# Kernel tuning notes

Hardware: AMD Instinct MI355X
Metric: run time of the kernel (lower is better)

Reference implementation:

```python
import jax, jax.numpy as jnp
import numpy as np

TEMPERATURE = 1.0

N = 20000  # = subsample, so the random-subsample branch is not taken


def setup_inputs() -> dict:
    key = jax.random.key(0)
    k1, k2 = jax.random.split(key)
    logits = jax.random.normal(k1, (N,), dtype=jnp.float32)
    targets = jax.random.uniform(k2, (N,), dtype=jnp.float32)  # relevance in [0,1]
    return {"logits": logits, "targets": targets}


def reference(logits, targets):
    s = logits.reshape(-1)
    y = targets.reshape(-1)
    n = s.shape[0]
    t = jnp.asarray(TEMPERATURE, dtype=s.dtype)

    # diff[i, j] = s[j] - s[i]; approx rank of item j = 1 + sum_i sigmoid((s[j]-s[i])/T)
    diff = s[None, :] - s[:, None]                     # [n, n]
    approx_rank = jax.nn.sigmoid(diff / t).sum(axis=0) + 1.0

    discount = 1.0 / jnp.log2(approx_rank + 1.0)
    dcg = jnp.sum(y * discount)

    ideal_rank = jnp.arange(1, n + 1, dtype=s.dtype)
    ideal_discount = 1.0 / jnp.log2(ideal_rank + 1.0)
    sorted_y = jnp.sort(y)[::-1]                        # descending
    idcg = jnp.sum(sorted_y * ideal_discount)

    ndcg = dcg / (idcg + 1e-8)
    loss = 1.0 - ndcg
    # early-return guard: if total relevance < 1, loss is 0
    return jnp.where(jnp.sum(y) < 1.0, jnp.zeros((), dtype=s.dtype), loss)
```

## Files before the change

kernel.cpp:

```cpp
#include <hip/hip_runtime.h>
#include <hip/hip_bf16.h>


#define LOG2E 1.442695040888963387f
#define M_NODES 64
#define XHALF 8.0
#define NB 2048
#define PI_D 3.14159265358979323846
#define BT 1024

#if __has_builtin(__builtin_amdgcn_exp2f)
#define EXP2(x) __builtin_amdgcn_exp2f(x)
#else
#define EXP2(x) exp2f(x)
#endif

#if __has_builtin(__builtin_amdgcn_rcpf)
#define RCP(x) __builtin_amdgcn_rcpf(x)
#else
#define RCP(x) (1.0f / (x))
#endif

#define OFF_ACC    0
#define OFF_DONE   32
#define OFF_PREFIX 64
#define OFF_NODES  8320
#define OFF_YBKT   8832

__device__ __forceinline__ int bucket_of(float y) {
  int b = (int)(y * (float)NB);
  return b < 0 ? 0 : (b > NB - 1 ? NB - 1 : b);
}

__global__ __launch_bounds__(BT) void produce_kernel(
    const float* __restrict__ s, const float* __restrict__ y,
    char* __restrict__ ws, int n) {
  const int tid = threadIdx.x;
  double* acc = (double*)(ws + OFF_ACC);
  int* done = (int*)(ws + OFF_DONE);
  int* prefix = (int*)(ws + OFF_PREFIX);
  float2* nodes = (float2*)(ws + OFF_NODES);
  float* ybkt = (float*)(ws + OFF_YBKT);

  if (blockIdx.x == 0) {
    __shared__ int hist[NB];
    __shared__ int part[BT];
    for (int b = tid; b < NB; b += BT) hist[b] = 0;
    __syncthreads();

    const float4* y4 = (const float4*)y;
    const int n4 = n >> 2;
    for (int i = tid; i < n4; i += BT) {
      const float4 v = y4[i];
      atomicAdd(&hist[bucket_of(v.x)], 1);
      atomicAdd(&hist[bucket_of(v.y)], 1);
      atomicAdd(&hist[bucket_of(v.z)], 1);
      atomicAdd(&hist[bucket_of(v.w)], 1);
    }
    for (int i = (n4 << 2) + tid; i < n; i += BT)
      atomicAdd(&hist[bucket_of(y[i])], 1);
    __syncthreads();

    const int base = tid * 2;
    const int l0 = hist[base], l1 = hist[base + 1];
    const int sum2 = l0 + l1;
    part[tid] = sum2;
    __syncthreads();
    for (int off = 1; off < BT; off <<= 1) {
      const int v = (tid >= off) ? part[tid - off] : 0;
      __syncthreads();
      part[tid] += v;
      __syncthreads();
    }
    const int run = part[tid] - sum2;
    prefix[base] = run;
    prefix[base + 1] = run + l0;
    if (tid == BT - 1) prefix[NB] = run + sum2;
    __syncthreads();
    hist[base] = run;
    hist[base + 1] = run + l0;
    __syncthreads();

    for (int i = tid; i < n4; i += BT) {
      const float4 v = y4[i];
      ybkt[atomicAdd(&hist[bucket_of(v.x)], 1)] = v.x;
      ybkt[atomicAdd(&hist[bucket_of(v.y)], 1)] = v.y;
      ybkt[atomicAdd(&hist[bucket_of(v.z)], 1)] = v.z;
      ybkt[atomicAdd(&hist[bucket_of(v.w)], 1)] = v.w;
    }
    for (int i = (n4 << 2) + tid; i < n; i += BT) {
      const float yv = y[i];
      ybkt[atomicAdd(&hist[bucket_of(yv)], 1)] = yv;
    }
  } else {
    const int k = blockIdx.x - 1;
    if (k == 0 && tid < 4) {
      if (tid < 3) acc[tid] = 0.0;
      else *done = 0;
    }
    const float xk =
        (float)(XHALF * cos(PI_D * (double)k / (double)(M_NODES - 1)));
    double F = 0.0;
    const float4* s4 = (const float4*)s;
    const int n4 = n >> 2;
    for (int i = tid; i < n4; i += BT) {
      const float4 v = s4[i];
      float t = RCP(1.0f + EXP2((v.x - xk) * LOG2E));
      t += RCP(1.0f + EXP2((v.y - xk) * LOG2E));
      t += RCP(1.0f + EXP2((v.z - xk) * LOG2E));
      t += RCP(1.0f + EXP2((v.w - xk) * LOG2E));
      F += (double)t;
    }
    for (int i = (n4 << 2) + tid; i < n; i += BT)
      F += (double)RCP(1.0f + EXP2((s[i] - xk) * LOG2E));
    for (int off = 32; off > 0; off >>= 1) F += __shfl_down(F, off);
    __shared__ double wsum[BT / 64];
    if ((tid & 63) == 0) wsum[tid >> 6] = F;
    __syncthreads();
    if (tid == 0) {
      double t = 0.0;
#pragma unroll
      for (int w = 0; w < BT / 64; ++w) t += wsum[w];
      nodes[k] = make_float2(xk, (float)t);
    }
  }
}

__global__ __launch_bounds__(256) void consume_kernel(
    const float* __restrict__ s, const float* __restrict__ y,
    char* __restrict__ ws, float* __restrict__ out, int n, int nblocks) {
  double* acc = (double*)(ws + OFF_ACC);
  int* done = (int*)(ws + OFF_DONE);
  const int* prefix = (const int*)(ws + OFF_PREFIX);
  const float2* nodes = (const float2*)(ws + OFF_NODES);
  const float* ybkt = (const float*)(ws + OFF_YBKT);

  __shared__ float2 nd[M_NODES];
  __shared__ double wsum[12];
  const int tid = threadIdx.x;
  if (tid < M_NODES) nd[tid] = nodes[tid];
  __syncthreads();

  const int j = blockIdx.x * 256 + tid;
  double dc = 0.0, ic = 0.0, ys = 0.0;
  if (j < n) {
    const float x = s[j];
    const float yj = y[j];
    double num = 0.0, den = 0.0;
    int hit = -1;
#pragma unroll
    for (int k = 0; k < M_NODES; ++k) {
      const float d = x - nd[k].x;
      float w = (k & 1) ? -1.0f : 1.0f;
      if (k == 0 || k == M_NODES - 1) w *= 0.5f;
      if (d == 0.0f) {
        hit = k;
      } else {
        const float iv = w * RCP(d);
        num += (double)iv * (double)nd[k].y;
        den += (double)iv;
      }
    }
    const double F = (hit >= 0) ? (double)nd[hit].y : (num / den);

    const int b = bucket_of(yj);
    const int s1 = prefix[b + 1];
    int cnt = n - s1;
    for (int t = prefix[b]; t < s1; ++t) cnt += (ybkt[t] > yj);

    dc = (double)yj / log2(F + 2.0);
    ic = (double)yj / log2((double)cnt + 2.0);
    ys = (double)yj;
  }
  for (int off = 32; off > 0; off >>= 1) {
    dc += __shfl_down(dc, off);
    ic += __shfl_down(ic, off);
    ys += __shfl_down(ys, off);
  }
  const int wv = tid >> 6;
  if ((tid & 63) == 0) {
    wsum[wv] = dc;
    wsum[wv + 4] = ic;
    wsum[wv + 8] = ys;
  }
  __syncthreads();
  if (tid == 0) {
    atomicAdd(&acc[0], wsum[0] + wsum[1] + wsum[2] + wsum[3]);
    atomicAdd(&acc[1], wsum[4] + wsum[5] + wsum[6] + wsum[7]);
    atomicAdd(&acc[2], wsum[8] + wsum[9] + wsum[10] + wsum[11]);
    __threadfence();
    const int old = atomicAdd(done, 1);
    if (old == nblocks - 1) {
      const double dcg = atomicAdd(&acc[0], 0.0);
      const double idcg = atomicAdd(&acc[1], 0.0);
      const double ysum = atomicAdd(&acc[2], 0.0);
      const double loss = 1.0 - dcg / (idcg + 1e-8);
      out[0] = (ysum < 1.0) ? 0.0f : (float)loss;
    }
  }
}

extern "C" void kernel_launch(void* const* d_in, const int* in_sizes, int n_in,
                              void* d_out, int out_size, void* d_ws, size_t ws_size,
                              hipStream_t stream) {
  const float* s = (const float*)d_in[0];
  const float* y = (const float*)d_in[1];
  const int n = in_sizes[0];
  char* wsb = (char*)d_ws;

  const int nb = (n + 255) / 256;
  produce_kernel<<<M_NODES + 1, BT, 0, stream>>>(s, y, wsb, n);
  consume_kernel<<<nb, 256, 0, stream>>>(s, y, wsb, (float*)d_out, n, nb);
}
```

Baseline: 82.61 us.

## Fuse produce and consume kernels with a software grid barrier

Merges the two launches into one kernel of 65 blocks of 1024 threads that meet at a global atomic spin barrier. After the barrier, each block computes NDCG terms for 1024 items, reading node values and the bucketed histogram through relaxed atomic loads. Workspace state moves into device globals, which the last block resets for the next call. This removes one kernel launch and the gap between launches. The barrier relies on all 65 blocks being co-resident, and the consume phase now only covers n up to 65*1024 items.

```diff
diff --git a/kernel.cpp b/kernel.cpp
--- a/kernel.cpp
+++ b/kernel.cpp
@@ -1,5 +1,4 @@
 #include <hip/hip_runtime.h>
-#include <hip/hip_bf16.h>
 
 
 #define LOG2E 1.442695040888963387f
@@ -8,6 +7,8 @@
 #define NB 2048
 #define PI_D 3.14159265358979323846
 #define BT 1024
+#define GBLKS (M_NODES + 1)
+#define MAXN 131072
 
 #if __has_builtin(__builtin_amdgcn_exp2f)
 #define EXP2(x) __builtin_amdgcn_exp2f(x)
@@ -21,30 +22,38 @@
 #define RCP(x) (1.0f / (x))
 #endif
 
-#define OFF_ACC    0
-#define OFF_DONE   32
-#define OFF_PREFIX 64
-#define OFF_NODES  8320
-#define OFF_YBKT   8832
+__device__ double g_acc[3] = {0.0, 0.0, 0.0};
+__device__ int g_done = 0;
+__device__ int g_bar = 0;
+__device__ int g_prefix[NB + 1];
+__device__ float g_nodex[M_NODES];
+__device__ float g_nodef[M_NODES];
+__device__ float g_ybkt[MAXN];
 
 __device__ __forceinline__ int bucket_of(float y) {
   int b = (int)(y * (float)NB);
   return b < 0 ? 0 : (b > NB - 1 ? NB - 1 : b);
 }
 
-__global__ __launch_bounds__(BT) void produce_kernel(
+__device__ __forceinline__ float aloadf(const float* p) {
+  return __hip_atomic_load(p, __ATOMIC_RELAXED, __HIP_MEMORY_SCOPE_AGENT);
+}
+__device__ __forceinline__ int aloadi(const int* p) {
+  return __hip_atomic_load(p, __ATOMIC_RELAXED, __HIP_MEMORY_SCOPE_AGENT);
+}
+
+__global__ __launch_bounds__(BT) void fused_kernel(
     const float* __restrict__ s, const float* __restrict__ y,
-    char* __restrict__ ws, int n) {
+    float* __restrict__ out, int n) {
   const int tid = threadIdx.x;
-  double* acc = (double*)(ws + OFF_ACC);
-  int* done = (int*)(ws + OFF_DONE);
-  int* prefix = (int*)(ws + OFF_PREFIX);
-  float2* nodes = (float2*)(ws + OFF_NODES);
-  float* ybkt = (float*)(ws + OFF_YBKT);
-
-  if (blockIdx.x == 0) {
-    __shared__ int hist[NB];
-    __shared__ int part[BT];
+  const int blk = blockIdx.x;
+
+  __shared__ int hist[NB];
+  __shared__ int part[BT];
+  __shared__ double wsum[48];
+  __shared__ float2 nd[M_NODES];
+
+  if (blk == 0) {
     for (int b = tid; b < NB; b += BT) hist[b] = 0;
     __syncthreads();
 
@@ -73,9 +82,9 @@
       __syncthreads();
     }
     const int run = part[tid] - sum2;
-    prefix[base] = run;
-    prefix[base + 1] = run + l0;
-    if (tid == BT - 1) prefix[NB] = run + sum2;
+    g_prefix[base] = run;
+    g_prefix[base + 1] = run + l0;
+    if (tid == BT - 1) g_prefix[NB] = run + sum2;
     __syncthreads();
     hist[base] = run;
     hist[base + 1] = run + l0;
@@ -83,21 +92,17 @@
 
     for (int i = tid; i < n4; i += BT) {
       const float4 v = y4[i];
-      ybkt[atomicAdd(&hist[bucket_of(v.x)], 1)] = v.x;
-      ybkt[atomicAdd(&hist[bucket_of(v.y)], 1)] = v.y;
-      ybkt[atomicAdd(&hist[bucket_of(v.z)], 1)] = v.z;
-      ybkt[atomicAdd(&hist[bucket_of(v.w)], 1)] = v.w;
+      g_ybkt[atomicAdd(&hist[bucket_of(v.x)], 1)] = v.x;
+      g_ybkt[atomicAdd(&hist[bucket_of(v.y)], 1)] = v.y;
+      g_ybkt[atomicAdd(&hist[bucket_of(v.z)], 1)] = v.z;
+      g_ybkt[atomicAdd(&hist[bucket_of(v.w)], 1)] = v.w;
     }
     for (int i = (n4 << 2) + tid; i < n; i += BT) {
       const float yv = y[i];
-      ybkt[atomicAdd(&hist[bucket_of(yv)], 1)] = yv;
+      g_ybkt[atomicAdd(&hist[bucket_of(yv)], 1)] = yv;
     }
   } else {
-    const int k = blockIdx.x - 1;
-    if (k == 0 && tid < 4) {
-      if (tid < 3) acc[tid] = 0.0;
-      else *done = 0;
-    }
+    const int k = blk - 1;
     const float xk =
         (float)(XHALF * cos(PI_D * (double)k / (double)(M_NODES - 1)));
     double F = 0.0;
@@ -114,34 +119,31 @@
     for (int i = (n4 << 2) + tid; i < n; i += BT)
       F += (double)RCP(1.0f + EXP2((s[i] - xk) * LOG2E));
     for (int off = 32; off > 0; off >>= 1) F += __shfl_down(F, off);
-    __shared__ double wsum[BT / 64];
     if ((tid & 63) == 0) wsum[tid >> 6] = F;
     __syncthreads();
     if (tid == 0) {
       double t = 0.0;
 #pragma unroll
       for (int w = 0; w < BT / 64; ++w) t += wsum[w];
-      nodes[k] = make_float2(xk, (float)t);
-    }
-  }
-}
-
-__global__ __launch_bounds__(256) void consume_kernel(
-    const float* __restrict__ s, const float* __restrict__ y,
-    char* __restrict__ ws, float* __restrict__ out, int n, int nblocks) {
-  double* acc = (double*)(ws + OFF_ACC);
-  int* done = (int*)(ws + OFF_DONE);
-  const int* prefix = (const int*)(ws + OFF_PREFIX);
-  const float2* nodes = (const float2*)(ws + OFF_NODES);
-  const float* ybkt = (const float*)(ws + OFF_YBKT);
-
-  __shared__ float2 nd[M_NODES];
-  __shared__ double wsum[12];
-  const int tid = threadIdx.x;
-  if (tid < M_NODES) nd[tid] = nodes[tid];
+      g_nodex[k] = xk;
+      g_nodef[k] = (float)t;
+    }
+  }
+
+  if (tid == 0) {
+    __threadfence();
+    atomicAdd(&g_bar, 1);
+    while (__hip_atomic_load(&g_bar, __ATOMIC_ACQUIRE,
+                             __HIP_MEMORY_SCOPE_AGENT) < GBLKS)
+      __builtin_amdgcn_s_sleep(2);
+  }
   __syncthreads();
 
-  const int j = blockIdx.x * 256 + tid;
+  if (tid < M_NODES)
+    nd[tid] = make_float2(aloadf(&g_nodex[tid]), aloadf(&g_nodef[tid]));
+  __syncthreads();
+
+  const int j = blk * BT + tid;
   double dc = 0.0, ic = 0.0, ys = 0.0;
   if (j < n) {
     const float x = s[j];
@@ -164,9 +166,10 @@
     const double F = (hit >= 0) ? (double)nd[hit].y : (num / den);
 
     const int b = bucket_of(yj);
-    const int s1 = prefix[b + 1];
+    const int s0 = aloadi(&g_prefix[b]);
+    const int s1 = aloadi(&g_prefix[b + 1]);
     int cnt = n - s1;
-    for (int t = prefix[b]; t < s1; ++t) cnt += (ybkt[t] > yj);
+    for (int t = s0; t < s1; ++t) cnt += (aloadf(&g_ybkt[t]) > yj);
 
     dc = (double)yj / log2(F + 2.0);
     ic = (double)yj / log2((double)cnt + 2.0);
@@ -180,35 +183,46 @@
   const int wv = tid >> 6;
   if ((tid & 63) == 0) {
     wsum[wv] = dc;
-    wsum[wv + 4] = ic;
-    wsum[wv + 8] = ys;
+    wsum[wv + 16] = ic;
+    wsum[wv + 32] = ys;
   }
   __syncthreads();
   if (tid == 0) {
-    atomicAdd(&acc[0], wsum[0] + wsum[1] + wsum[2] + wsum[3]);
-    atomicAdd(&acc[1], wsum[4] + wsum[5] + wsum[6] + wsum[7]);
-    atomicAdd(&acc[2], wsum[8] + wsum[9] + wsum[10] + wsum[11]);
+    double a = 0.0, b2 = 0.0, c = 0.0;
+#pragma unroll
+    for (int w = 0; w < 16; ++w) {
+      a += wsum[w];
+      b2 += wsum[w + 16];
+      c += wsum[w + 32];
+    }
+    atomicAdd(&g_acc[0], a);
+    atomicAdd(&g_acc[1], b2);
+    atomicAdd(&g_acc[2], c);
     __threadfence();
-    const int old = atomicAdd(done, 1);
-    if (old == nblocks - 1) {
-      const double dcg = atomicAdd(&acc[0], 0.0);
-      const double idcg = atomicAdd(&acc[1], 0.0);
-      const double ysum = atomicAdd(&acc[2], 0.0);
+    const int old = atomicAdd(&g_done, 1);
+    if (old == GBLKS - 1) {
+      const double dcg = atomicAdd(&g_acc[0], 0.0);
+      const double idcg = atomicAdd(&g_acc[1], 0.0);
+      const double yss = atomicAdd(&g_acc[2], 0.0);
       const double loss = 1.0 - dcg / (idcg + 1e-8);
-      out[0] = (ysum < 1.0) ? 0.0f : (float)loss;
+      out[0] = (yss < 1.0) ? 0.0f : (float)loss;
+      g_acc[0] = 0.0;
+      g_acc[1] = 0.0;
+      g_acc[2] = 0.0;
+      g_done = 0;
+      __threadfence();
+      __hip_atomic_store(&g_bar, 0, __ATOMIC_RELEASE, __HIP_MEMORY_SCOPE_AGENT);
     }
   }
 }
 
 extern "C" void kernel_launch(void* const* d_in, const int* in_sizes, int n_in,
-                              void* d_out, int out_size, void* d_ws, size_t ws_size,
-                              hipStream_t stream) {
+                              void* d_out, int out_size, void* d_ws,
+                              size_t ws_size, hipStream_t stream) {
   const float* s = (const float*)d_in[0];
   const float* y = (const float*)d_in[1];
   const int n = in_sizes[0];
-  char* wsb = (char*)d_ws;
-
-  const int nb = (n + 255) / 256;
-  produce_kernel<<<M_NODES + 1, BT, 0, stream>>>(s, y, wsb, n);
-  consume_kernel<<<nb, 256, 0, stream>>>(s, y, wsb, (float*)d_out, n, nb);
-}
+  (void)d_ws;
+  (void)ws_size;
+  fused_kernel<<<GBLKS, BT, 0, stream>>>(s, y, (float*)d_out, n);
+}
```

Measured after the change: 106.6 us. +29.0%, slower.
